# Optimization experiments

Measured on AMD Instinct MI355X. Metric: run time of the kernel, lower is better.

Reference implementation:

```python
import jax, jax.numpy as jnp
import numpy as np

B, GRID, IN_CO, OUT_CO = 32, 4096, 64, 64
T_EMB, N_MODES = 256, 512
M_HALF = N_MODES // 2 + 1  # 257 retained rFFT modes


def setup_inputs() -> dict:
    key = jax.random.key(0)
    ks = jax.random.split(key, 6)
    w_std = jnp.sqrt(1.0 / (2.0 * IN_CO))
    return {
        "x": jax.random.normal(ks[0], (B, GRID, IN_CO), jnp.float32),
        "t_emb": jax.random.normal(ks[1], (B, T_EMB), jnp.float32),
        "weights_real": jax.random.normal(ks[2], (M_HALF, IN_CO, OUT_CO), jnp.float32) * w_std,
        "weights_imag": jax.random.normal(ks[3], (M_HALF, IN_CO, OUT_CO), jnp.float32) * w_std,
        "dense_real": jax.random.normal(ks[4], (T_EMB, M_HALF), jnp.float32) * jnp.sqrt(1.0 / T_EMB),
        "dense_imag": jax.random.normal(ks[5], (T_EMB, M_HALF), jnp.float32) * jnp.sqrt(1.0 / T_EMB),
    }


def reference(x, t_emb, weights_real, weights_imag, dense_real, dense_imag):
    b, in_grid_sz, _ = x.shape
    m = weights_real.shape[0]  # n_modes//2 + 1
    weights = weights_real + 1j * weights_imag  # (m, in_co, out_co)
    # rFFT over the grid axis
    x_ft = jnp.fft.rfft(x, axis=-2, norm="forward")  # (b, grid//2+1, in_co) complex
    # time modulation per mode: Dense(real) + i*Dense(imag)
    t_tr = (t_emb @ dense_real) + 1j * (t_emb @ dense_imag)  # (b, m)
    # original einsum with eye == elementwise per-mode scale then per-mode matmul
    x_out = jnp.einsum("bmi,mio->bmo", x_ft[:, :m, :], weights) * t_tr[:, :, None]
    out_ft = jnp.zeros((b, in_grid_sz // 2 + 1, weights.shape[-1]), jnp.complex64)
    out_ft = out_ft.at[:, :m, :].set(x_out)
    return jnp.fft.irfft(out_ft, axis=-2, n=in_grid_sz, norm="forward")
```

## Files before the change

kernel.cpp:

```cpp
#include <hip/hip_runtime.h>
#include <hip/hip_bf16.h>

typedef short short8 __attribute__((ext_vector_type(8)));
typedef float f32x4 __attribute__((ext_vector_type(4)));
typedef const void __attribute__((address_space(1))) as1_void;
typedef void __attribute__((address_space(3))) as3_void;

__device__ __forceinline__ float sin_rev(float r) {
  float o; asm("v_sin_f32 %0, %1" : "=v"(o) : "v"(r)); return o;
}
__device__ __forceinline__ float cos_rev(float r) {
  float o; asm("v_cos_f32 %0, %1" : "=v"(o) : "v"(r)); return o;
}

#define INV4096 0.000244140625f
#define INV16   0.0625f

__global__ __launch_bounds__(256) void prep_kernel(__hip_bfloat16* __restrict__ F2,
                                                   __hip_bfloat16* __restrict__ Gm2,
                                                   const float* __restrict__ t_emb,
                                                   const float* __restrict__ dr,
                                                   const float* __restrict__ di,
                                                   float* __restrict__ Sr,
                                                   float* __restrict__ Si,
                                                   const float* __restrict__ x,
                                                   __hip_bfloat16* __restrict__ E,
                                                   __hip_bfloat16* __restrict__ O,
                                                   float* __restrict__ Xr256p,
                                                   float* __restrict__ x2048f,
                                                   const float* __restrict__ Wr,
                                                   const float* __restrict__ Wi,
                                                   __hip_bfloat16* __restrict__ Wb) {
  const int bid = blockIdx.x;
  const int tid = threadIdx.x;
  __shared__ float te[256];
  __shared__ float tileA[64][65];
  __shared__ float tileB[64][65];
  __shared__ float red[4][64];
  __shared__ float xm[64];

  if (bid < 512) {
    const int row = bid;
    const int m   = (row < 256) ? row : (row - 255);
    const bool is_cos = (row < 256);
    int n0 = tid * 8;
    union { short8 v; unsigned short u[8]; } pk;
#pragma unroll
    for (int j = 0; j < 8; ++j) {
      int ph = (m * (n0 + j)) & 4095;
      float v = is_cos ?  cos_rev((float)ph * INV4096)
                       : -sin_rev((float)ph * INV4096);
      __hip_bfloat16 h = __float2bfloat16(v);
      pk.u[j] = *(unsigned short*)&h;
    }
    *(short8*)&F2[(size_t)row * 2048 + n0] = pk.v;
  } else if (bid < 1024) {
    const int gb = bid - 512;
    int e  = tid * 8;
    int n  = gb * 4 + (e >> 9);
    int c0 = e & 511;
    union { short8 v; unsigned short u[8]; } pk;
#pragma unroll
    for (int j = 0; j < 8; ++j) {
      int cc = c0 + j;
      int k  = (cc < 256) ? cc : (cc - 255);
      int ph = (n * k) & 4095;
      float v = (cc < 256) ? cos_rev((float)ph * INV4096)
                           : sin_rev((float)ph * INV4096);
      __hip_bfloat16 h = __float2bfloat16(v);
      pk.u[j] = *(unsigned short*)&h;
    }
    *(short8*)&Gm2[(size_t)n * 512 + c0] = pk.v;
  } else if (bid < 1056) {
    int b = bid - 1024;
    te[tid] = t_emb[b * 256 + tid];
    __syncthreads();
    for (int m = tid; m < 257; m += 256) {
      float ar = 0.f, ai = 0.f;
      for (int t = 0; t < 256; ++t) {
        float e = te[t];
        ar += e * dr[t * 257 + m];
        ai += e * di[t * 257 + m];
      }
      float c = (m == 0 ? 1.0f : 2.0f) * (1.0f / 4096.0f);
      Sr[b * 257 + m] = ar * c;
      Si[b * 257 + m] = ai * c;
    }
  } else if (bid < 2080) {
    int idx = bid - 1056;
    int nt = idx & 31;
    int b  = idx >> 5;
    int n0 = nt * 64;
    int m0r = (63 - nt) * 64;
#pragma unroll
    for (int it = 0; it < 4; ++it) {
      int c = it * 256 + tid;
      int r = c >> 4, i4 = (c & 15) * 4;
      float4 v = *(const float4*)&x[((size_t)b * 4096 + n0 + r) * 64 + i4];
      tileA[r][i4 + 0] = v.x; tileA[r][i4 + 1] = v.y;
      tileA[r][i4 + 2] = v.z; tileA[r][i4 + 3] = v.w;
      float4 w = *(const float4*)&x[((size_t)b * 4096 + m0r + r) * 64 + i4];
      tileB[r][i4 + 0] = w.x; tileB[r][i4 + 1] = w.y;
      tileB[r][i4 + 2] = w.z; tileB[r][i4 + 3] = w.w;
    }
    if (tid < 64) xm[tid] = (nt > 0) ? x[((size_t)b * 4096 + (4096 - n0)) * 64 + tid] : 0.f;
    __syncthreads();
#pragma unroll
    for (int it = 0; it < 2; ++it) {
      int c  = it * 256 + tid;
      int i  = c >> 3;
      int ch = c & 7;
      union { short8 v; unsigned short u[8]; } pe, po;
#pragma unroll
      for (int jj = 0; jj < 8; ++jj) {
        int j = ch * 8 + jj;
        float a = tileA[j][i];
        float mir = (j == 0) ? xm[i] : tileB[64 - j][i];
        __hip_bfloat16 he = __float2bfloat16(a + mir);
        __hip_bfloat16 ho = __float2bfloat16(a - mir);
        pe.u[jj] = *(unsigned short*)&he;
        po.u[jj] = *(unsigned short*)&ho;
      }
      size_t base = ((size_t)b * 64 + i) * 2048 + n0 + ch * 8;
      *(short8*)&E[base] = pe.v;
      *(short8*)&O[base] = po.v;
    }
    {
      int i = tid & 63, g = tid >> 6;
      float acc = 0.f;
#pragma unroll
      for (int j = 0; j < 16; ++j) {
        float w = cos_rev((float)j * INV16);
        acc += w * (tileA[g * 16 + j][i] + tileB[g * 16 + j][i]);
      }
      red[g][i] = acc;
    }
    __syncthreads();
    if (tid < 64) {
      Xr256p[((size_t)b * 32 + nt) * 64 + tid] =
          red[0][tid] + red[1][tid] + red[2][tid] + red[3][tid];
      if (nt == 31) x2048f[b * 64 + tid] = tileB[0][tid];
    }
  } else {
    int idx  = bid - 2080;
    int k    = idx >> 2;
    int quad = idx & 3;
    const float* src = (quad < 2) ? (Wr + (size_t)k * 4096 + quad * 2048)
                                  : (Wi + (size_t)k * 4096 + (quad - 2) * 2048);
    __hip_bfloat16* dst = Wb + (size_t)k * 8192 + (quad < 2 ? quad * 2048 : 4096 + (quad - 2) * 2048);
    int e = tid * 8;
    float4 v0 = *(const float4*)&src[e];
    float4 v1 = *(const float4*)&src[e + 4];
    union { short8 v; unsigned short u[8]; } pk;
    float vv[8] = {v0.x, v0.y, v0.z, v0.w, v1.x, v1.y, v1.z, v1.w};
#pragma unroll
    for (int j = 0; j < 8; ++j) {
      __hip_bfloat16 h = __float2bfloat16(vv[j]);
      pk.u[j] = *(unsigned short*)&h;
    }
    *(short8*)&dst[e] = pk.v;
  }
}

template <int NF>
__device__ __forceinline__ void stage_tileT(const __hip_bfloat16* __restrict__ A, int lda, int m0,
                                            const __hip_bfloat16* __restrict__ B, int ldb, int n0,
                                            int kt, __hip_bfloat16* As, __hip_bfloat16* Bs,
                                            int tid) {
#pragma unroll
  for (int j = 0; j < 4; ++j) {
    int c   = j * 256 + tid;
    int row = c >> 3;
    int chg = (c & 7) ^ (row & 7);
    const __hip_bfloat16* ga = A + (size_t)(m0 + row) * lda + kt + chg * 8;
    __hip_bfloat16* la = As + (size_t)(j * 256 + (tid & 192)) * 8;
    __builtin_amdgcn_global_load_lds((as1_void*)ga, (as3_void*)la, 16, 0, 0);
  }
#pragma unroll
  for (int j = 0; j < NF; ++j) {
    int c   = j * 256 + tid;
    int row = c >> 3;
    int chg = (c & 7) ^ (row & 7);
    const __hip_bfloat16* gb = B + (size_t)(n0 + row) * ldb + kt + chg * 8;
    __hip_bfloat16* lb = Bs + (size_t)(j * 256 + (tid & 192)) * 8;
    __builtin_amdgcn_global_load_lds((as1_void*)gb, (as3_void*)lb, 16, 0, 0);
  }
}

template <int NF>
__device__ __forceinline__ void compute_stepT(const __hip_bfloat16* As, const __hip_bfloat16* Bs,
                                              int wr, int wc, int fr, int fq,
                                              f32x4 acc[4][NF]) {
#pragma unroll
  for (int kk = 0; kk < 2; ++kk) {
    short8 av[4], bv[NF];
#pragma unroll
    for (int m = 0; m < 4; ++m) {
      int row  = wr + m * 16 + fr;
      int slot = (fq + kk * 4) ^ (row & 7);
      av[m] = *(const short8*)(As + row * 64 + slot * 8);
    }
#pragma unroll
    for (int n = 0; n < NF; ++n) {
      int row  = wc + n * 16 + fr;
      int slot = (fq + kk * 4) ^ (row & 7);
      bv[n] = *(const short8*)(Bs + row * 64 + slot * 8);
    }
#pragma unroll
    for (int m = 0; m < 4; ++m)
#pragma unroll
      for (int n = 0; n < NF; ++n)
        acc[m][n] = __builtin_amdgcn_mfma_f32_16x16x32_bf16(av[m], bv[n], acc[m][n], 0, 0, 0);
  }
}

template <int NF>
__device__ __forceinline__ void gemm_coreT(const __hip_bfloat16* __restrict__ A, int lda, int m0,
                                           const __hip_bfloat16* __restrict__ B, int ldb, int n0,
                                           int k0, int ksteps,
                                           __hip_bfloat16* As, __hip_bfloat16* Bs,
                                           f32x4 acc[4][NF]) {
  const int tid  = threadIdx.x;
  const int lane = tid & 63;
  const int wv   = tid >> 6;
  const int wr   = (wv >> 1) * 64;
  const int wc   = (wv & 1) * (NF * 16);
  const int fr   = lane & 15;
  const int fq   = lane >> 4;

  for (int ks = 0; ks < ksteps; ++ks) {
    stage_tileT<NF>(A, lda, m0, B, ldb, n0, k0 + ks * 64, As, Bs, tid);
    __syncthreads();
    compute_stepT<NF>(As, Bs, wr, wc, fr, fq, acc);
    __syncthreads();
  }
}

__global__ __launch_bounds__(256) void gemm1_kernel(const __hip_bfloat16* __restrict__ F2,
                                                    const __hip_bfloat16* __restrict__ E,
                                                    const __hip_bfloat16* __restrict__ O,
                                                    __hip_bfloat16* __restrict__ C1, int kchunk) {
  __shared__ __hip_bfloat16 As[128 * 64];
  __shared__ __hip_bfloat16 Bs[128 * 64];
  int n0 = blockIdx.x * 128;
  int m0 = blockIdx.y * 128;
  int k0 = blockIdx.z * kchunk;
  const __hip_bfloat16* B = (m0 < 256) ? E : O;
  f32x4 acc[4][4];
#pragma unroll
  for (int m = 0; m < 4; ++m)
#pragma unroll
    for (int n = 0; n < 4; ++n)
#pragma unroll
      for (int r = 0; r < 4; ++r) acc[m][n][r] = 0.f;

  gemm_coreT<4>(F2, 2048, m0, B, 2048, n0, k0, kchunk >> 6, As, Bs, acc);

  const int lane = threadIdx.x & 63;
  const int wv   = threadIdx.x >> 6;
  const int wr   = (wv >> 1) * 64, wc = (wv & 1) * 64;
  const int fr   = lane & 15, fq = lane >> 4;
  __hip_bfloat16* P = C1 + (size_t)blockIdx.z * (512 * 2048);
#pragma unroll
  for (int m = 0; m < 4; ++m)
#pragma unroll
    for (int n = 0; n < 4; ++n)
#pragma unroll
      for (int j = 0; j < 4; ++j) {
        int row = m0 + wr + m * 16 + fq * 4 + j;
        int col = n0 + wc + n * 16 + fr;
        P[(size_t)row * 2048 + col] = __float2bfloat16(acc[m][n][j]);
      }
}

__global__ __launch_bounds__(256) void mix_kernel(const __hip_bfloat16* __restrict__ C1,
                                                  const float* __restrict__ Xr256p,
                                                  const float* __restrict__ x2048f,
                                                  const __hip_bfloat16* __restrict__ Wb,
                                                  const float* __restrict__ Sr,
                                                  const float* __restrict__ Si,
                                                  __hip_bfloat16* __restrict__ Y2T,
                                                  __hip_bfloat16* __restrict__ Yx,
                                                  int splitk) {
  const int k = blockIdx.x;
  const int q = blockIdx.y;
  const int tid = threadIdx.x;
  __shared__ float wlr[4096];
  __shared__ float wli[4096];
  __shared__ float xs2[2][1024];
  __shared__ float xs[1024];

  const __hip_bfloat16* wbg = Wb + (size_t)k * 8192;
  for (int c = tid; c < 1024; c += 256) {
    short8 v = *(const short8*)(wbg + c * 8);
    float* dst = (c < 512) ? &wlr[c * 8] : &wli[(c - 512) * 8];
#pragma unroll
    for (int j = 0; j < 8; ++j) {
      unsigned short u = (unsigned short)v[j];
      dst[j] = __bfloat162float(*(__hip_bfloat16*)&u);
    }
  }

  const size_t PST = 512ull * 2048;
  if (k < 256) {
    const int zg   = tid >> 7;
    const int part = (tid >> 6) & 1;
    const int ln   = tid & 63;
    const int row  = (part == 0) ? k : 255 + k;
    float f[8] = {0.f, 0.f, 0.f, 0.f, 0.f, 0.f, 0.f, 0.f};
    if (part == 0 || k > 0) {
      const __hip_bfloat16* src = C1 + (size_t)row * 2048 + q * 512 + ln * 8;
      const int zh = splitk >> 1;
      for (int z = zg * zh; z < zg * zh + zh; ++z) {
        short8 v = *(const short8*)(src + (size_t)z * PST);
#pragma unroll
        for (int j = 0; j < 8; ++j) {
          unsigned short u = (unsigned short)v[j];
          f[j] += __bfloat162float(*(__hip_bfloat16*)&u);
        }
      }
    }
    if (part == 0 && zg == 0) {
      float par = (k & 1) ? -1.f : 1.f;
#pragma unroll
      for (int j = 0; j < 8; ++j) f[j] += par * x2048f[q * 512 + ln * 8 + j];
    }
#pragma unroll
    for (int j = 0; j < 8; ++j) xs2[zg][part * 512 + ln * 8 + j] = f[j];
    __syncthreads();
    for (int e = tid; e < 1024; e += 256) xs[e] = xs2[0][e] + xs2[1][e];
  } else {
    for (int idx = tid; idx < 1024; idx += 256) {
      int part = idx >> 9;
      int c    = idx & 511;
      float s = 0.f;
      if (part == 0) {
        int bi = q * 512 + c;
        const float* sp = Xr256p + (size_t)(bi >> 6) * 2048 + (bi & 63);
#pragma unroll 8
        for (int nt = 0; nt < 32; ++nt) s += sp[nt * 64];
      } else {
        const __hip_bfloat16* src = C1 + (size_t)511 * 2048 + q * 512 + c;
        for (int z = 0; z < splitk; ++z) s += __bfloat162float(src[(size_t)z * PST]);
      }
      xs[idx] = s;
    }
    __syncthreads();
  }
  __syncthreads();

  const int o  = tid & 63;
  const int jj = tid >> 6;
  const int bl0 = jj * 2, bl1 = jj * 2 + 1;
  float pr0 = 0.f, pi0 = 0.f, pr1 = 0.f, pi1 = 0.f;
#pragma unroll 8
  for (int i = 0; i < 64; ++i) {
    float wrv = wlr[i * 64 + o];
    float wiv = wli[i * 64 + o];
    float xr0 = xs[bl0 * 64 + i], xi0 = xs[512 + bl0 * 64 + i];
    float xr1 = xs[bl1 * 64 + i], xi1 = xs[512 + bl1 * 64 + i];
    pr0 += xr0 * wrv - xi0 * wiv;
    pi0 += xr0 * wiv + xi0 * wrv;
    pr1 += xr1 * wrv - xi1 * wiv;
    pi1 += xr1 * wiv + xi1 * wrv;
  }
  int b0 = q * 8 + bl0, b1 = q * 8 + bl1;
  float sr0 = Sr[b0 * 257 + k], si0 = Si[b0 * 257 + k];
  float sr1 = Sr[b1 * 257 + k], si1 = Si[b1 * 257 + k];
  int bo0 = b0 * 64 + o, bo1 = b1 * 64 + o;
  __hip_bfloat16 yr0 = __float2bfloat16(pr0 * sr0 - pi0 * si0);
  __hip_bfloat16 yi0 = __float2bfloat16(pr0 * si0 + pi0 * sr0);
  __hip_bfloat16 yr1 = __float2bfloat16(pr1 * sr1 - pi1 * si1);
  __hip_bfloat16 yi1 = __float2bfloat16(pr1 * si1 + pi1 * sr1);
  if (k < 256) {
    Y2T[(size_t)bo0 * 512 + k] = yr0;
    Y2T[(size_t)bo1 * 512 + k] = yr1;
  } else {
    Yx[bo0] = yr0;
    Yx[bo1] = yr1;
  }
  if (k >= 1) {
    Y2T[(size_t)bo0 * 512 + 255 + k] = yi0;
    Y2T[(size_t)bo1 * 512 + 255 + k] = yi1;
  }
}

__global__ __launch_bounds__(256) void gemm2_kernel(const __hip_bfloat16* __restrict__ Gm2,
                                                    const __hip_bfloat16* __restrict__ Y2T,
                                                    const __hip_bfloat16* __restrict__ Yx,
                                                    float* __restrict__ out) {
  __shared__ __hip_bfloat16 As[128 * 64];
  __shared__ __hip_bfloat16 Bs[64 * 64];
  __shared__ float red2[4][64];
  int n0 = blockIdx.x * 64;
  int m0 = blockIdx.y * 128;
  f32x4 accC[4][2], accS[4][2];
#pragma unroll
  for (int m = 0; m < 4; ++m)
#pragma unroll
    for (int n = 0; n < 2; ++n)
#pragma unroll
      for (int r = 0; r < 4; ++r) { accC[m][n][r] = 0.f; accS[m][n][r] = 0.f; }

  gemm_coreT<2>(Gm2, 512, m0, Y2T, 512, n0, 0,   4, As, Bs, accC);
  gemm_coreT<2>(Gm2, 512, m0, Y2T, 512, n0, 256, 4, As, Bs, accS);

  const int lane = threadIdx.x & 63;
  const int wv   = threadIdx.x >> 6;
  const int wr   = (wv >> 1) * 64, wc = (wv & 1) * 32;
  const int fr   = lane & 15, fq = lane >> 4;
  float yx[2];
#pragma unroll
  for (int n = 0; n < 2; ++n)
    yx[n] = __bfloat162float(Yx[n0 + wc + n * 16 + fr]);
#pragma unroll
  for (int m = 0; m < 4; ++m)
#pragma unroll
    for (int j = 0; j < 4; ++j) {
      int row = m0 + wr + m * 16 + fq * 4 + j;
      float g = cos_rev((float)(row & 15) * INV16);
#pragma unroll
      for (int n = 0; n < 2; ++n) {
        int col = n0 + wc + n * 16 + fr;
        int b = col >> 6, o = col & 63;
        float vC = accC[m][n][j] + g * yx[n];
        float vS = accS[m][n][j];
        out[((size_t)b * 4096 + row) * 64 + o] = vC - vS;
        if (row > 0)
          out[((size_t)b * 4096 + (4096 - row)) * 64 + o] = vC + vS;
      }
    }

  if (m0 == 0) {
    __syncthreads();
    const int tid = threadIdx.x;
    int col = tid & 63, grp = tid >> 6;
    int bo = n0 + col;
    float s = 0.f;
    for (int k = grp * 64; k < grp * 64 + 64; ++k) {
      float v = __bfloat162float(Y2T[(size_t)bo * 512 + k]);
      s += (k & 1) ? -v : v;
    }
    red2[grp][col] = s;
    __syncthreads();
    if (tid < 64) {
      int bo2 = n0 + tid;
      float alt = red2[0][tid] + red2[1][tid] + red2[2][tid] + red2[3][tid]
                + __bfloat162float(Yx[bo2]);
      int b = bo2 >> 6, o = bo2 & 63;
      out[((size_t)b * 4096 + 2048) * 64 + o] = alt;
    }
  }
}

extern "C" void kernel_launch(void* const* d_in, const int* in_sizes, int n_in,
                              void* d_out, int out_size, void* d_ws, size_t ws_size,
                              hipStream_t stream) {
  const float* x  = (const float*)d_in[0];
  const float* te = (const float*)d_in[1];
  const float* wr = (const float*)d_in[2];
  const float* wi = (const float*)d_in[3];
  const float* dr = (const float*)d_in[4];
  const float* di = (const float*)d_in[5];
  float* out = (float*)d_out;

  char* p = (char*)d_ws;
  auto alloc = [&](size_t bytes) -> char* {
    char* r = p;
    p += (bytes + 255) & ~(size_t)255;
    return r;
  };
  __hip_bfloat16* F2  = (__hip_bfloat16*)alloc(512ull * 2048 * 2);
  __hip_bfloat16* Gm2 = (__hip_bfloat16*)alloc(2048ull * 512 * 2);
  __hip_bfloat16* E   = (__hip_bfloat16*)alloc(2048ull * 2048 * 2);
  __hip_bfloat16* O   = (__hip_bfloat16*)alloc(2048ull * 2048 * 2);
  float* Xr256p = (float*)alloc(32ull * 32 * 64 * 4);
  float* x2048f = (float*)alloc(2048 * 4);
  float* Sr = (float*)alloc(32 * 257 * 4);
  float* Si = (float*)alloc(32 * 257 * 4);
  __hip_bfloat16* Y2T = (__hip_bfloat16*)alloc(2048ull * 512 * 2);
  __hip_bfloat16* Yx  = (__hip_bfloat16*)alloc(2048 * 2);
  __hip_bfloat16* Wb  = (__hip_bfloat16*)alloc(257ull * 8192 * 2);
  size_t fixed = (size_t)(p - (char*)d_ws);

  int splitk = 2;
  if (ws_size >= fixed + 8ull * 512 * 2048 * 2)      splitk = 8;
  else if (ws_size >= fixed + 4ull * 512 * 2048 * 2) splitk = 4;
  __hip_bfloat16* C1 = (__hip_bfloat16*)alloc((size_t)splitk * 512 * 2048 * 2);
  int kchunk = 2048 / splitk;

  prep_kernel<<<3108, 256, 0, stream>>>(F2, Gm2, te, dr, di, Sr, Si, x, E, O,
                                        Xr256p, x2048f, wr, wi, Wb);
  gemm1_kernel<<<dim3(16, 4, splitk), 256, 0, stream>>>(F2, E, O, C1, kchunk);
  mix_kernel<<<dim3(257, 4), 256, 0, stream>>>(C1, Xr256p, x2048f, Wb, Sr, Si, Y2T, Yx, splitk);
  gemm2_kernel<<<dim3(32, 16), 256, 0, stream>>>(Gm2, Y2T, Yx, out);
}
```

Measured before the change: 88.87 us.

## Interleave split-K partials per row and halve mix kernel grid with 16 batches per block

The split-K partial layout in gemm1 changes so that each row's partials sit next to each other in memory (row*splitk+z), letting the mix kernel read them as contiguous chunks. The mix kernel now runs on a 257x2 grid, with each block covering 16 batches instead of 8. Each block therefore loads the per-mode weight tile into LDS once for twice as much work, and the inner product reuses each weight load across 4 batches. In exchange the grid is half the size (514 blocks), which lowers parallelism, and the gemm1 stores become more strided.

Result: faster. 84.88 us (median of 2 runs) (-4.5%).

```diff
diff --git a/kernel.cpp b/kernel.cpp
--- a/kernel.cpp
+++ b/kernel.cpp
@@ -239,7 +239,8 @@
 __global__ __launch_bounds__(256) void gemm1_kernel(const __hip_bfloat16* __restrict__ F2,
                                                     const __hip_bfloat16* __restrict__ E,
                                                     const __hip_bfloat16* __restrict__ O,
-                                                    __hip_bfloat16* __restrict__ C1, int kchunk) {
+                                                    __hip_bfloat16* __restrict__ C1,
+                                                    int kchunk, int splitk) {
   __shared__ __hip_bfloat16 As[128 * 64];
   __shared__ __hip_bfloat16 Bs[128 * 64];
   int n0 = blockIdx.x * 128;
@@ -260,7 +261,6 @@
   const int wv   = threadIdx.x >> 6;
   const int wr   = (wv >> 1) * 64, wc = (wv & 1) * 64;
   const int fr   = lane & 15, fq = lane >> 4;
-  __hip_bfloat16* P = C1 + (size_t)blockIdx.z * (512 * 2048);
 #pragma unroll
   for (int m = 0; m < 4; ++m)
 #pragma unroll
@@ -269,7 +269,7 @@
       for (int j = 0; j < 4; ++j) {
         int row = m0 + wr + m * 16 + fq * 4 + j;
         int col = n0 + wc + n * 16 + fr;
-        P[(size_t)row * 2048 + col] = __float2bfloat16(acc[m][n][j]);
+        C1[((size_t)row * splitk + blockIdx.z) * 2048 + col] = __float2bfloat16(acc[m][n][j]);
       }
 }
 
@@ -287,8 +287,7 @@
   const int tid = threadIdx.x;
   __shared__ float wlr[4096];
   __shared__ float wli[4096];
-  __shared__ float xs2[2][1024];
-  __shared__ float xs[1024];
+  __shared__ float xs[2048];
 
   const __hip_bfloat16* wbg = Wb + (size_t)k * 8192;
   for (int c = tid; c < 1024; c += 256) {
@@ -301,87 +300,79 @@
     }
   }
 
-  const size_t PST = 512ull * 2048;
-  if (k < 256) {
-    const int zg   = tid >> 7;
-    const int part = (tid >> 6) & 1;
-    const int ln   = tid & 63;
-    const int row  = (part == 0) ? k : 255 + k;
+  {
+    const int part = tid >> 7;
+    const int ln   = tid & 127;
+    const int bi0  = q * 1024 + ln * 8;
     float f[8] = {0.f, 0.f, 0.f, 0.f, 0.f, 0.f, 0.f, 0.f};
-    if (part == 0 || k > 0) {
-      const __hip_bfloat16* src = C1 + (size_t)row * 2048 + q * 512 + ln * 8;
-      const int zh = splitk >> 1;
-      for (int z = zg * zh; z < zg * zh + zh; ++z) {
-        short8 v = *(const short8*)(src + (size_t)z * PST);
-#pragma unroll
-        for (int j = 0; j < 8; ++j) {
-          unsigned short u = (unsigned short)v[j];
-          f[j] += __bfloat162float(*(__hip_bfloat16*)&u);
+    if (k < 256) {
+      if (part == 0 || k > 0) {
+        int row = part ? 255 + k : k;
+        const __hip_bfloat16* src = C1 + (size_t)row * splitk * 2048 + bi0;
+        for (int z = 0; z < splitk; ++z) {
+          short8 v = *(const short8*)(src + (size_t)z * 2048);
+#pragma unroll
+          for (int j = 0; j < 8; ++j) {
+            unsigned short u = (unsigned short)v[j];
+            f[j] += __bfloat162float(*(__hip_bfloat16*)&u);
+          }
         }
       }
-    }
-    if (part == 0 && zg == 0) {
-      float par = (k & 1) ? -1.f : 1.f;
-#pragma unroll
-      for (int j = 0; j < 8; ++j) f[j] += par * x2048f[q * 512 + ln * 8 + j];
-    }
-#pragma unroll
-    for (int j = 0; j < 8; ++j) xs2[zg][part * 512 + ln * 8 + j] = f[j];
-    __syncthreads();
-    for (int e = tid; e < 1024; e += 256) xs[e] = xs2[0][e] + xs2[1][e];
-  } else {
-    for (int idx = tid; idx < 1024; idx += 256) {
-      int part = idx >> 9;
-      int c    = idx & 511;
-      float s = 0.f;
       if (part == 0) {
-        int bi = q * 512 + c;
-        const float* sp = Xr256p + (size_t)(bi >> 6) * 2048 + (bi & 63);
+        float par = (k & 1) ? -1.f : 1.f;
+#pragma unroll
+        for (int j = 0; j < 8; ++j) f[j] += par * x2048f[bi0 + j];
+      }
+    } else {
+      if (part == 0) {
+        const float* sp = Xr256p + (size_t)(bi0 >> 6) * 2048 + (bi0 & 63);
 #pragma unroll 8
-        for (int nt = 0; nt < 32; ++nt) s += sp[nt * 64];
+        for (int nt = 0; nt < 32; ++nt)
+#pragma unroll
+          for (int j = 0; j < 8; ++j) f[j] += sp[nt * 64 + j];
       } else {
-        const __hip_bfloat16* src = C1 + (size_t)511 * 2048 + q * 512 + c;
-        for (int z = 0; z < splitk; ++z) s += __bfloat162float(src[(size_t)z * PST]);
-      }
-      xs[idx] = s;
-    }
-    __syncthreads();
+        const __hip_bfloat16* src = C1 + (size_t)511 * splitk * 2048 + bi0;
+        for (int z = 0; z < splitk; ++z) {
+          short8 v = *(const short8*)(src + (size_t)z * 2048);
+#pragma unroll
+          for (int j = 0; j < 8; ++j) {
+            unsigned short u = (unsigned short)v[j];
+            f[j] += __bfloat162float(*(__hip_bfloat16*)&u);
+          }
+        }
+      }
+    }
+#pragma unroll
+    for (int j = 0; j < 8; ++j) xs[part * 1024 + ln * 8 + j] = f[j];
   }
   __syncthreads();
 
   const int o  = tid & 63;
   const int jj = tid >> 6;
-  const int bl0 = jj * 2, bl1 = jj * 2 + 1;
-  float pr0 = 0.f, pi0 = 0.f, pr1 = 0.f, pi1 = 0.f;
-#pragma unroll 8
+  float pr[4] = {0.f, 0.f, 0.f, 0.f};
+  float pi[4] = {0.f, 0.f, 0.f, 0.f};
+#pragma unroll 4
   for (int i = 0; i < 64; ++i) {
     float wrv = wlr[i * 64 + o];
     float wiv = wli[i * 64 + o];
-    float xr0 = xs[bl0 * 64 + i], xi0 = xs[512 + bl0 * 64 + i];
-    float xr1 = xs[bl1 * 64 + i], xi1 = xs[512 + bl1 * 64 + i];
-    pr0 += xr0 * wrv - xi0 * wiv;
-    pi0 += xr0 * wiv + xi0 * wrv;
-    pr1 += xr1 * wrv - xi1 * wiv;
-    pi1 += xr1 * wiv + xi1 * wrv;
-  }
-  int b0 = q * 8 + bl0, b1 = q * 8 + bl1;
-  float sr0 = Sr[b0 * 257 + k], si0 = Si[b0 * 257 + k];
-  float sr1 = Sr[b1 * 257 + k], si1 = Si[b1 * 257 + k];
-  int bo0 = b0 * 64 + o, bo1 = b1 * 64 + o;
-  __hip_bfloat16 yr0 = __float2bfloat16(pr0 * sr0 - pi0 * si0);
-  __hip_bfloat16 yi0 = __float2bfloat16(pr0 * si0 + pi0 * sr0);
-  __hip_bfloat16 yr1 = __float2bfloat16(pr1 * sr1 - pi1 * si1);
-  __hip_bfloat16 yi1 = __float2bfloat16(pr1 * si1 + pi1 * sr1);
-  if (k < 256) {
-    Y2T[(size_t)bo0 * 512 + k] = yr0;
-    Y2T[(size_t)bo1 * 512 + k] = yr1;
-  } else {
-    Yx[bo0] = yr0;
-    Yx[bo1] = yr1;
-  }
-  if (k >= 1) {
-    Y2T[(size_t)bo0 * 512 + 255 + k] = yi0;
-    Y2T[(size_t)bo1 * 512 + 255 + k] = yi1;
+#pragma unroll
+    for (int u = 0; u < 4; ++u) {
+      int lb = (jj * 4 + u) * 64 + i;
+      float xr = xs[lb], xi = xs[1024 + lb];
+      pr[u] += xr * wrv - xi * wiv;
+      pi[u] += xr * wiv + xi * wrv;
+    }
+  }
+#pragma unroll
+  for (int u = 0; u < 4; ++u) {
+    int b = q * 16 + jj * 4 + u;
+    float sr = Sr[b * 257 + k], si = Si[b * 257 + k];
+    int bo = b * 64 + o;
+    __hip_bfloat16 yr = __float2bfloat16(pr[u] * sr - pi[u] * si);
+    __hip_bfloat16 yi = __float2bfloat16(pr[u] * si + pi[u] * sr);
+    if (k < 256) Y2T[(size_t)bo * 512 + k] = yr;
+    else         Yx[bo] = yr;
+    if (k >= 1)  Y2T[(size_t)bo * 512 + 255 + k] = yi;
   }
 }
 
@@ -491,7 +482,7 @@
 
   prep_kernel<<<3108, 256, 0, stream>>>(F2, Gm2, te, dr, di, Sr, Si, x, E, O,
                                         Xr256p, x2048f, wr, wi, Wb);
-  gemm1_kernel<<<dim3(16, 4, splitk), 256, 0, stream>>>(F2, E, O, C1, kchunk);
-  mix_kernel<<<dim3(257, 4), 256, 0, stream>>>(C1, Xr256p, x2048f, Wb, Sr, Si, Y2T, Yx, splitk);
+  gemm1_kernel<<<dim3(16, 4, splitk), 256, 0, stream>>>(F2, E, O, C1, kchunk, splitk);
+  mix_kernel<<<dim3(257, 2), 256, 0, stream>>>(C1, Xr256p, x2048f, Wb, Sr, Si, Y2T, Yx, splitk);
   gemm2_kernel<<<dim3(32, 16), 256, 0, stream>>>(Gm2, Y2T, Yx, out);
 }
```
